# Optimization experiments

Hardware: AMD Instinct MI355X
Metric: run time of the kernel (lower is better)

Reference implementation:

```python
import jax, jax.numpy as jnp
import numpy as np

N_NODES = 50000
N_EDGES = 800000
D = 256          # in_features == out_features == num_classes
T = 4            # number of replicas / linear heads
NS = 64          # num_edges (hyperedges)


def setup_inputs() -> dict:
    key = jax.random.key(0)
    ks = jax.random.split(key, 10)
    s = D ** -0.5
    return {
        "edge_index": jax.random.randint(ks[0], (2, N_EDGES), 0, N_NODES, dtype=jnp.int64)
        if jax.config.jax_enable_x64 else jax.random.randint(ks[0], (2, N_EDGES), 0, N_NODES, dtype=jnp.int32),
        "features": jax.random.normal(ks[1], (N_NODES, D), jnp.float32),
        "lin_w": jax.random.normal(ks[2], (T, D, D), jnp.float32) * s,
        "lin_b": jax.random.normal(ks[3], (T, D), jnp.float32) * 0.01,
        "gcn0_w": jax.random.normal(ks[4], (D, D), jnp.float32) * s,
        "gcn0_b": jax.random.normal(ks[5], (D,), jnp.float32) * 0.01,
        "gcn1_w": jax.random.normal(ks[6], (D, D), jnp.float32) * s,
        "gcn1_b": jax.random.normal(ks[7], (D,), jnp.float32) * 0.01,
        "lin1_w": jax.random.normal(ks[8], (D, NS), jnp.float32) * s,
        "lin1_b": jax.random.normal(ks[9], (NS,), jnp.float32) * 0.01,
    }


def _l2_normalize(x, eps=1e-8):
    n = jnp.sqrt(jnp.sum(x * x, axis=-1, keepdims=True))
    return x / jnp.maximum(n, eps)


def reference(edge_index, features, lin_w, lin_b, gcn0_w, gcn0_b, gcn1_w, gcn1_b, lin1_w, lin1_b):
    num_nodes, d = features.shape
    t = lin_w.shape[0]
    ns = lin1_w.shape[1]
    scale = d ** -0.5  # out_features ** -0.5

    # t linear projections: (t, N, D)
    transformed = jnp.einsum('nd,tdk->tnk', features, lin_w) + lin_b[:, None, :]

    src, dst = edge_index[0], edge_index[1]
    # cosine similarity of features[src] vs each replica's transformed[dst]
    fs = _l2_normalize(features)[src]              # (E, D)
    tf_n = _l2_normalize(transformed)              # (t, N, D)
    sim = jnp.stack([jnp.sum(fs * tf_n[i][dst], axis=-1) for i in range(t)], axis=1)  # (E, t)
    best_idx = jnp.argmax(sim, axis=1)
    best_dst = dst + best_idx.astype(dst.dtype) * num_nodes

    # extra per-replica identity edges: node n -> node n + i*N, i in [0, t)
    ar = jnp.arange(num_nodes, dtype=src.dtype)
    extra_src = jnp.tile(ar, t)
    extra_dst = (ar[None, :] + (jnp.arange(t, dtype=src.dtype) * num_nodes)[:, None]).reshape(-1)

    src_all = jnp.concatenate([src, src, extra_src])
    dst_all = jnp.concatenate([dst, best_dst, extra_dst])
    n_total = (t + 1) * num_nodes

    # PyG gcn_norm: drop pre-existing self loops (weight 0), add one self loop per node,
    # symmetric normalization with degree from destination index.
    loops = jnp.arange(n_total, dtype=src.dtype)
    src2 = jnp.concatenate([src_all, loops])
    dst2 = jnp.concatenate([dst_all, loops])
    w2 = jnp.concatenate([jnp.where(src_all == dst_all, 0.0, 1.0).astype(features.dtype),
                          jnp.ones(n_total, features.dtype)])
    deg = jax.ops.segment_sum(w2, dst2, num_segments=n_total)
    dinv = jnp.where(deg > 0, jax.lax.rsqrt(deg), 0.0)
    norm = w2 * dinv[src2] * dinv[dst2]

    def gcn(x, W, b):
        xw = x @ W
        return jax.ops.segment_sum(norm[:, None] * xw[src2], dst2, num_segments=n_total) + b

    all_features = jnp.concatenate([features, transformed.reshape(t * num_nodes, d)], axis=0)
    # dropout is identity in eval mode
    h = jax.nn.relu(all_features)
    h = gcn(h, gcn0_w, gcn0_b)
    h = jax.nn.relu(h)
    all_features2 = gcn(h, gcn1_w, gcn1_b)          # ((t+1)N, D)
    logits = jax.nn.relu(all_features2) @ lin1_w + lin1_b  # ((t+1)N, NS)

    # H[n, c] counts how many of the (t+1) replicas assign node n to cluster c
    classes = jnp.argmax(logits.reshape(t + 1, num_nodes, ns), axis=-1)  # (t+1, N)
    H = jax.nn.one_hot(classes, ns, dtype=features.dtype).sum(axis=0)     # (N, NS)

    # hyperedge features: sum of all_features2 over base-replica nodes in each hyperedge
    mask = (H > 0).astype(features.dtype)                                  # (N, NS)
    hyperedge_features = mask.T @ all_features2[:num_nodes]                # (NS, D)

    dots = (all_features @ hyperedge_features.T) * scale                   # ((t+1)N, NS)
    return H, hyperedge_features, dots
```

## Files before the change

kernel.cpp:

```cpp
#include <hip/hip_runtime.h>

#define D 256
#define T 4
#define NS 64

typedef unsigned int uint32;
typedef short s16x8 __attribute__((ext_vector_type(8)));
typedef float f32x4 __attribute__((ext_vector_type(4)));

__device__ __forceinline__ float bflo(uint32 u) { return __uint_as_float(u << 16); }
__device__ __forceinline__ float bfhi(uint32 u) { return __uint_as_float(u & 0xffff0000u); }
__device__ __forceinline__ unsigned short f2bf(float x) {
    uint32 u = __float_as_uint(x);
    u = u + 0x7FFFu + ((u >> 16) & 1u);
    return (unsigned short)(u >> 16);
}
__device__ __forceinline__ uint32 pack2(float a, float b) {
    return (uint32)f2bf(a) | ((uint32)f2bf(b) << 16);
}
__device__ __forceinline__ uint32 relu2(uint32 u) {
    uint32 s = u & 0x80008000u;
    uint32 m = ((s >> 15) ^ 0x00010001u) * 0xFFFFu;
    return u & m;
}

__global__ void zero_kernel(uint32* __restrict__ p, long long n)
{
    long long i = (long long)blockIdx.x * blockDim.x + threadIdx.x;
    long long st = (long long)gridDim.x * blockDim.x;
    for (; i < n; i += st) p[i] = 0u;
}

__global__ void f2bf_kernel(const float* __restrict__ in, unsigned short* __restrict__ out,
                            long long n8)
{
    long long i = (long long)blockIdx.x * blockDim.x + threadIdx.x;
    long long st = (long long)gridDim.x * blockDim.x;
    for (; i < n8; i += st) {
        float4 a = *(const float4*)(in + i * 8);
        float4 b = *(const float4*)(in + i * 8 + 4);
        uint4 o;
        o.x = pack2(a.x, a.y); o.y = pack2(a.z, a.w);
        o.z = pack2(b.x, b.y); o.w = pack2(b.z, b.w);
        *(uint4*)(out + i * 8) = o;
    }
}

__global__ void wfrag_kernel(const float* __restrict__ g0, const float* __restrict__ g1,
                             const float* __restrict__ lw, unsigned short* __restrict__ out)
{
    int o = blockIdx.x * 256 + threadIdx.x;
    int mat = blockIdx.y;
    const float* W = (mat == 0) ? g0 : (mat == 1) ? g1 : (lw + (size_t)(mat - 2) * 65536);
    int j = o & 7, lane = (o >> 3) & 63, ks = (o >> 9) & 7, nt = o >> 12;
    int n15 = lane & 15, quad = lane >> 4;
    int k = ks * 32 + quad * 8 + j;
    int n = nt * 16 + n15;
    out[(size_t)mat * 65536 + o] = f2bf(W[(size_t)k * 256 + n]);
}

__global__ __launch_bounds__(256, 2)
void gemm_mfma(const unsigned short* __restrict__ A,
               const unsigned short* __restrict__ Wfrag,
               const float* __restrict__ bias,
               unsigned short* __restrict__ Cout,
               int M, int nStripes)
{
    __shared__ unsigned short Asm[64 * 264];
    int t = threadIdx.x, w = t >> 6, lane = t & 63;
    int n15 = lane & 15, quad = lane >> 4;
    int z = blockIdx.y;
    Wfrag += (size_t)z * 65536;
    bias  += (size_t)z * 256;
    Cout  += (size_t)z * (size_t)M * 256;

    s16x8 bfr[4][8];
#pragma unroll
    for (int nt = 0; nt < 4; nt++)
#pragma unroll
        for (int ks = 0; ks < 8; ks++)
            bfr[nt][ks] = *(const s16x8*)(Wfrag +
                (size_t)(((w * 4 + nt) * 8 + ks) * 64 + lane) * 8);

    float bcol[4];
#pragma unroll
    for (int nt = 0; nt < 4; nt++) bcol[nt] = bias[(w * 4 + nt) * 16 + n15];

    for (int s = blockIdx.x; s < nStripes; s += gridDim.x) {
        int m0 = s * 64;
        __syncthreads();
#pragma unroll
        for (int i = 0; i < 8; i++) {
            int idx = i * 256 + t;
            int m = idx >> 5, kc = (idx & 31) * 8;
            int gm = m0 + m;
            uint4 v = make_uint4(0u, 0u, 0u, 0u);
            if (gm < M) v = *(const uint4*)(A + (size_t)gm * 256 + kc);
            *(uint4*)(Asm + m * 264 + kc) = v;
        }
        __syncthreads();

        f32x4 acc[4][4];
#pragma unroll
        for (int rt = 0; rt < 4; rt++)
#pragma unroll
            for (int nt = 0; nt < 4; nt++)
#pragma unroll
                for (int e = 0; e < 4; e++) acc[rt][nt][e] = 0.f;

#pragma unroll
        for (int rt = 0; rt < 4; rt++) {
            int abase = (rt * 16 + n15) * 264 + quad * 8;
#pragma unroll
            for (int ks = 0; ks < 8; ks++) {
                s16x8 a = *(const s16x8*)(Asm + abase + ks * 32);
#pragma unroll
                for (int nt = 0; nt < 4; nt++)
                    acc[rt][nt] = __builtin_amdgcn_mfma_f32_16x16x32_bf16(
                        a, bfr[nt][ks], acc[rt][nt], 0, 0, 0);
            }
        }

#pragma unroll
        for (int rt = 0; rt < 4; rt++) {
            int row0 = m0 + rt * 16 + quad * 4;
#pragma unroll
            for (int nt = 0; nt < 4; nt++) {
                int colp = (w * 4 + nt) * 16 + n15;
#pragma unroll
                for (int r = 0; r < 4; r++) {
                    int gr = row0 + r;
                    if (gr < M)
                        Cout[(size_t)gr * 256 + colp] = f2bf(acc[rt][nt][r] + bcol[nt]);
                }
            }
        }
    }
}

__global__ __launch_bounds__(256)
void tinv_kernel(const unsigned short* __restrict__ tr, float* __restrict__ tinv, int rows)
{
    int wave = threadIdx.x >> 6, lane = threadIdx.x & 63;
    int r = blockIdx.x * 4 + wave;
    if (r >= rows) return;
    uint2 q = *(const uint2*)(tr + (size_t)r * D + lane * 4);
    float a = bflo(q.x), b = bfhi(q.x), c = bflo(q.y), d = bfhi(q.y);
    float s = a * a + b * b + c * c + d * d;
#pragma unroll
    for (int off = 32; off; off >>= 1) s += __shfl_xor(s, off);
    if (lane == 0) tinv[r] = 1.f / fmaxf(sqrtf(s), 1e-8f);
}

__global__ void ehist_kernel(const int* __restrict__ dst, int* __restrict__ ecnt, int E)
{
    for (int e = blockIdx.x * blockDim.x + threadIdx.x; e < E;
         e += gridDim.x * blockDim.x)
        atomicAdd(ecnt + dst[e], 1);
}

__global__ void escatter_kernel(const int* __restrict__ src, const int* __restrict__ dst,
                                const int* __restrict__ eptr, int* __restrict__ efill,
                                uint2* __restrict__ esorted, int E)
{
    for (int e = blockIdx.x * blockDim.x + threadIdx.x; e < E;
         e += gridDim.x * blockDim.x) {
        int d = dst[e];
        int pos = eptr[d] + atomicAdd(efill + d, 1);
        esorted[pos] = make_uint2((uint32)src[e], (uint32)d);
    }
}

__global__ __launch_bounds__(256)
void sim3_kernel(const uint2* __restrict__ esorted,
                 const unsigned short* __restrict__ featb,
                 const unsigned short* __restrict__ tr, const float* __restrict__ tinv,
                 int* __restrict__ bestS, int E, int Nn)
{
    int w = threadIdx.x >> 6, lane = threadIdx.x & 63;
    int n15 = lane & 15, quad = lane >> 4;
    int base = (blockIdx.x * 4 + w) * 16;
    if (base >= E) return;
    int ei = min(base + n15, E - 1);
    uint2 se = esorted[ei];
    const unsigned short* arow = featb + (size_t)se.x * D + quad * 8;
    const unsigned short* brow = tr + (size_t)se.y * D + quad * 8;
    size_t rstride = (size_t)Nn * D;

    f32x4 a0 = {0.f, 0.f, 0.f, 0.f}, a1 = a0, a2 = a0, a3 = a0;
#pragma unroll
    for (int ks = 0; ks < 8; ks++) {
        s16x8 a  = *(const s16x8*)(arow + ks * 32);
        s16x8 b0 = *(const s16x8*)(brow + ks * 32);
        s16x8 b1 = *(const s16x8*)(brow + rstride + ks * 32);
        s16x8 b2 = *(const s16x8*)(brow + 2 * rstride + ks * 32);
        s16x8 b3 = *(const s16x8*)(brow + 3 * rstride + ks * 32);
        a0 = __builtin_amdgcn_mfma_f32_16x16x32_bf16(a, b0, a0, 0, 0, 0);
        a1 = __builtin_amdgcn_mfma_f32_16x16x32_bf16(a, b1, a1, 0, 0, 0);
        a2 = __builtin_amdgcn_mfma_f32_16x16x32_bf16(a, b2, a2, 0, 0, 0);
        a3 = __builtin_amdgcn_mfma_f32_16x16x32_bf16(a, b3, a3, 0, 0, 0);
    }
    if (quad == (n15 >> 2) && base + n15 < E) {
        int r = n15 & 3;
        int d = (int)se.y;
        float v0 = a0[r] * tinv[d];
        float v1 = a1[r] * tinv[Nn + d];
        float v2 = a2[r] * tinv[2 * Nn + d];
        float v3 = a3[r] * tinv[3 * Nn + d];
        float bv = v0; int bi = 0;
        if (v1 > bv) { bv = v1; bi = 1; }
        if (v2 > bv) { bv = v2; bi = 2; }
        if (v3 > bv) { bv = v3; bi = 3; }
        bestS[base + n15] = bi;
    }
}

__device__ __forceinline__ void decode_edge(int e, const uint2* __restrict__ esorted,
                                            const int* __restrict__ bestS,
                                            int E, int Nn, int& s, int& d, bool& keep)
{
    if (e < E) {
        uint2 se = esorted[e];
        s = (int)se.x; d = (int)se.y; keep = (s != d);
    } else if (e < 2 * E) {
        int k = e - E;
        uint2 se = esorted[k];
        s = (int)se.x; d = (int)se.y + bestS[k] * Nn; keep = (s != d);
    } else if (e < 2 * E + T * Nn) {
        int k = e - 2 * E; int i = k / Nn; int n = k - i * Nn;
        s = n; d = n + i * Nn; keep = (i != 0);
    } else {
        int v = e - (2 * E + T * Nn); s = v; d = v; keep = true;
    }
}

__global__ void hist_kernel(const uint2* __restrict__ esorted, const int* __restrict__ bestS,
                            int* __restrict__ cnt, int E, int Nn)
{
    int total = 2 * E + (2 * T + 1) * Nn;
    for (int e = blockIdx.x * blockDim.x + threadIdx.x; e < total;
         e += gridDim.x * blockDim.x) {
        int s, d; bool keep;
        decode_edge(e, esorted, bestS, E, Nn, s, d, keep);
        if (keep) atomicAdd(cnt + d, 1);
    }
}

__global__ void dinv_kernel(const int* __restrict__ cnt, float* __restrict__ dinv, int n)
{
    int v = blockIdx.x * blockDim.x + threadIdx.x;
    if (v < n) dinv[v] = (cnt[v] > 0) ? rsqrtf((float)cnt[v]) : 0.f;
}

__global__ void emeta_kernel(const uint2* __restrict__ esorted, const int* __restrict__ bestS,
                             const float* __restrict__ dinv, uint2* __restrict__ emeta, int E)
{
    for (int e = blockIdx.x * blockDim.x + threadIdx.x; e < E;
         e += gridDim.x * blockDim.x) {
        uint2 se = esorted[e];
        uint32 packed = se.x | ((uint32)bestS[e] << 27);
        emeta[e] = make_uint2(packed, __float_as_uint(dinv[se.x]));
    }
}

__global__ void scan_sums(const int* __restrict__ cnt, int* __restrict__ aux, int n)
{
    __shared__ int sd[256];
    int idx = blockIdx.x * 256 + threadIdx.x;
    sd[threadIdx.x] = (idx < n) ? cnt[idx] : 0;
    __syncthreads();
    for (int off = 128; off; off >>= 1) {
        if (threadIdx.x < off) sd[threadIdx.x] += sd[threadIdx.x + off];
        __syncthreads();
    }
    if (threadIdx.x == 0) aux[blockIdx.x] = sd[0];
}

__global__ void scan_aux(const int* __restrict__ aux, int* __restrict__ auxex, int nb)
{
    __shared__ int sd[1024];
    int t = threadIdx.x;
    int v = (t < nb) ? aux[t] : 0;
    sd[t] = v;
    __syncthreads();
    for (int off = 1; off < 1024; off <<= 1) {
        int x = (t >= off) ? sd[t - off] : 0;
        __syncthreads();
        sd[t] += x;
        __syncthreads();
    }
    if (t < nb) auxex[t] = sd[t] - v;
}

__global__ void scan_write(const int* __restrict__ cnt, const int* __restrict__ auxex,
                           int* __restrict__ rowptr, int n)
{
    __shared__ int sd[256];
    int t = threadIdx.x;
    int idx = blockIdx.x * 256 + t;
    int v = (idx < n) ? cnt[idx] : 0;
    sd[t] = v;
    __syncthreads();
    for (int off = 1; off < 256; off <<= 1) {
        int x = (t >= off) ? sd[t - off] : 0;
        __syncthreads();
        sd[t] += x;
        __syncthreads();
    }
    if (idx < n) {
        int rp = auxex[blockIdx.x] + sd[t] - v;
        rowptr[idx] = rp;
        if (idx == n - 1) rowptr[n] = rp + v;
    }
}

__global__ __launch_bounds__(256)
void agg5_kernel(const int* __restrict__ eptr, const uint2* __restrict__ emeta,
                 const unsigned short* __restrict__ xa,
                 const unsigned short* __restrict__ xb,
                 const float* __restrict__ dinv,
                 unsigned short* __restrict__ outb, int Nn)
{
    int wave = threadIdx.x >> 6, lane = threadIdx.x & 63;
    int v = blockIdx.x * 4 + wave;
    if (v >= Nn) return;

    float dv  = dinv[v];
    float dr1 = dinv[v + Nn];
    float dr2 = dinv[v + 2 * Nn];
    float dr3 = dinv[v + 3 * Nn];
    float dr4 = dinv[v + 4 * Nn];

    uint2 qv = *(const uint2*)(xa + (size_t)v * D + lane * 4);
    qv.x = relu2(qv.x); qv.y = relu2(qv.y);
    float y0 = bflo(qv.x), y1 = bfhi(qv.x), y2 = bflo(qv.y), y3 = bfhi(qv.y);

    float wsb = dv * dv;
    float b0 = wsb * y0, b1 = wsb * y1, b2 = wsb * y2, b3 = wsb * y3;

    float wi1 = dv * dr1, wi2 = dv * dr2, wi3 = dv * dr3;
    float r10 = wi1 * y0, r11 = wi1 * y1, r12 = wi1 * y2, r13 = wi1 * y3;
    float r20 = wi2 * y0, r21 = wi2 * y1, r22 = wi2 * y2, r23 = wi2 * y3;
    float r30 = wi3 * y0, r31 = wi3 * y1, r32 = wi3 * y2, r33 = wi3 * y3;
    float r40 = 0.f, r41 = 0.f, r42 = 0.f, r43 = 0.f;

    {
        uint2 q = *(const uint2*)(xb + ((size_t)0 * Nn + v) * D + lane * 4);
        q.x = relu2(q.x); q.y = relu2(q.y);
        float ws = dr1 * dr1;
        r10 = fmaf(ws, bflo(q.x), r10); r11 = fmaf(ws, bfhi(q.x), r11);
        r12 = fmaf(ws, bflo(q.y), r12); r13 = fmaf(ws, bfhi(q.y), r13);
    }
    {
        uint2 q = *(const uint2*)(xb + ((size_t)1 * Nn + v) * D + lane * 4);
        q.x = relu2(q.x); q.y = relu2(q.y);
        float ws = dr2 * dr2;
        r20 = fmaf(ws, bflo(q.x), r20); r21 = fmaf(ws, bfhi(q.x), r21);
        r22 = fmaf(ws, bflo(q.y), r22); r23 = fmaf(ws, bfhi(q.y), r23);
    }
    {
        uint2 q = *(const uint2*)(xb + ((size_t)2 * Nn + v) * D + lane * 4);
        q.x = relu2(q.x); q.y = relu2(q.y);
        float ws = dr3 * dr3;
        r30 = fmaf(ws, bflo(q.x), r30); r31 = fmaf(ws, bfhi(q.x), r31);
        r32 = fmaf(ws, bflo(q.y), r32); r33 = fmaf(ws, bfhi(q.y), r33);
    }
    {
        uint2 q = *(const uint2*)(xb + ((size_t)3 * Nn + v) * D + lane * 4);
        q.x = relu2(q.x); q.y = relu2(q.y);
        float ws = dr4 * dr4;
        r40 = fmaf(ws, bflo(q.x), r40); r41 = fmaf(ws, bfhi(q.x), r41);
        r42 = fmaf(ws, bflo(q.y), r42); r43 = fmaf(ws, bfhi(q.y), r43);
    }

    int j = eptr[v], jend = eptr[v + 1];

#define EDGE_BODY(qq, ss, bb, ww)                                                  \
    {                                                                              \
        float x0 = bflo(qq.x), x1 = bfhi(qq.x), x2 = bflo(qq.y), x3 = bfhi(qq.y);  \
        float wb = (ss != v) ? (ww) * dv : 0.f;                                    \
        if (bb == 0) wb += wb;                                                     \
        b0 = fmaf(wb, x0, b0); b1 = fmaf(wb, x1, b1);                              \
        b2 = fmaf(wb, x2, b2); b3 = fmaf(wb, x3, b3);                              \
        if (bb == 1) {                                                             \
            float wr = (ww) * dr1;                                                 \
            r10 = fmaf(wr, x0, r10); r11 = fmaf(wr, x1, r11);                      \
            r12 = fmaf(wr, x2, r12); r13 = fmaf(wr, x3, r13);                      \
        } else if (bb == 2) {                                                      \
            float wr = (ww) * dr2;                                                 \
            r20 = fmaf(wr, x0, r20); r21 = fmaf(wr, x1, r21);                      \
            r22 = fmaf(wr, x2, r22); r23 = fmaf(wr, x3, r23);                      \
        } else if (bb == 3) {                                                      \
            float wr = (ww) * dr3;                                                 \
            r30 = fmaf(wr, x0, r30); r31 = fmaf(wr, x1, r31);                      \
            r32 = fmaf(wr, x2, r32); r33 = fmaf(wr, x3, r33);                      \
        }                                                                          \
    }

    for (; j + 2 <= jend; j += 2) {
        uint2 m0 = emeta[j];
        uint2 m1 = emeta[j + 1];
        uint32 su0 = (uint32)__builtin_amdgcn_readfirstlane((int)m0.x);
        uint32 su1 = (uint32)__builtin_amdgcn_readfirstlane((int)m1.x);
        float ws0 = __uint_as_float((uint32)__builtin_amdgcn_readfirstlane((int)m0.y));
        float ws1 = __uint_as_float((uint32)__builtin_amdgcn_readfirstlane((int)m1.y));
        int s0 = (int)(su0 & 0x07FFFFFFu), bx0 = (int)(su0 >> 27);
        int s1 = (int)(su1 & 0x07FFFFFFu), bx1 = (int)(su1 >> 27);
        uint2 q0 = *(const uint2*)(xa + (size_t)s0 * D + lane * 4);
        uint2 q1 = *(const uint2*)(xa + (size_t)s1 * D + lane * 4);
        q0.x = relu2(q0.x); q0.y = relu2(q0.y);
        q1.x = relu2(q1.x); q1.y = relu2(q1.y);
        EDGE_BODY(q0, s0, bx0, ws0);
        EDGE_BODY(q1, s1, bx1, ws1);
    }
    if (j < jend) {
        uint2 m0 = emeta[j];
        uint32 su0 = (uint32)__builtin_amdgcn_readfirstlane((int)m0.x);
        float ws0 = __uint_as_float((uint32)__builtin_amdgcn_readfirstlane((int)m0.y));
        int s0 = (int)(su0 & 0x07FFFFFFu), bx0 = (int)(su0 >> 27);
        uint2 q0 = *(const uint2*)(xa + (size_t)s0 * D + lane * 4);
        q0.x = relu2(q0.x); q0.y = relu2(q0.y);
        EDGE_BODY(q0, s0, bx0, ws0);
    }
#undef EDGE_BODY

    uint2 o;
    o.x = pack2(b0, b1); o.y = pack2(b2, b3);
    *(uint2*)(outb + (size_t)v * D + lane * 4) = o;
    o.x = pack2(r10, r11); o.y = pack2(r12, r13);
    *(uint2*)(outb + ((size_t)v + Nn) * D + lane * 4) = o;
    o.x = pack2(r20, r21); o.y = pack2(r22, r23);
    *(uint2*)(outb + ((size_t)v + 2 * (size_t)Nn) * D + lane * 4) = o;
    o.x = pack2(r30, r31); o.y = pack2(r32, r33);
    *(uint2*)(outb + ((size_t)v + 3 * (size_t)Nn) * D + lane * 4) = o;
    o.x = pack2(r40, r41); o.y = pack2(r42, r43);
    *(uint2*)(outb + ((size_t)v + 4 * (size_t)Nn) * D + lane * 4) = o;
}

__global__ __launch_bounds__(256, 2)
void logits_mfma(const unsigned short* __restrict__ af2, const float* __restrict__ Wl,
                 const float* __restrict__ bl, float* __restrict__ H,
                 int M, int Nn, int nStripes)
{
    __shared__ unsigned short Asm[64 * 264];
    int t = threadIdx.x, w = t >> 6, lane = t & 63;
    int n15 = lane & 15, quad = lane >> 4;

    s16x8 bfr[4][8];
#pragma unroll
    for (int nt = 0; nt < 4; nt++)
#pragma unroll
        for (int ks = 0; ks < 8; ks++) {
            s16x8 f;
#pragma unroll
            for (int j = 0; j < 8; j++) {
                int k = ks * 32 + quad * 8 + j;
                f[j] = (short)f2bf(Wl[(size_t)k * NS + nt * 16 + n15]);
            }
            bfr[nt][ks] = f;
        }
    float bcol[4];
#pragma unroll
    for (int nt = 0; nt < 4; nt++) bcol[nt] = bl[nt * 16 + n15];

    for (int s = blockIdx.x; s < nStripes; s += gridDim.x) {
        int m0 = s * 64;
        __syncthreads();
#pragma unroll
        for (int i = 0; i < 8; i++) {
            int idx = i * 256 + t;
            int m = idx >> 5, kc = (idx & 31) * 8;
            int gm = m0 + m;
            uint4 v = make_uint4(0u, 0u, 0u, 0u);
            if (gm < M) {
                v = *(const uint4*)(af2 + (size_t)gm * 256 + kc);
                v.x = relu2(v.x); v.y = relu2(v.y);
                v.z = relu2(v.z); v.w = relu2(v.w);
            }
            *(uint4*)(Asm + m * 264 + kc) = v;
        }
        __syncthreads();

        f32x4 acc[4];
#pragma unroll
        for (int nt = 0; nt < 4; nt++)
#pragma unroll
            for (int e = 0; e < 4; e++) acc[nt][e] = 0.f;

        int abase = (w * 16 + n15) * 264 + quad * 8;
#pragma unroll
        for (int ks = 0; ks < 8; ks++) {
            s16x8 a = *(const s16x8*)(Asm + abase + ks * 32);
#pragma unroll
            for (int nt = 0; nt < 4; nt++)
                acc[nt] = __builtin_amdgcn_mfma_f32_16x16x32_bf16(
                    a, bfr[nt][ks], acc[nt], 0, 0, 0);
        }

#pragma unroll
        for (int e = 0; e < 4; e++) {
            float bv = acc[0][e] + bcol[0]; int bi = n15;
#pragma unroll
            for (int nt = 1; nt < 4; nt++) {
                float v = acc[nt][e] + bcol[nt];
                int c = nt * 16 + n15;
                if (v > bv) { bv = v; bi = c; }
            }
#pragma unroll
            for (int off = 1; off < 16; off <<= 1) {
                float ov = __shfl_xor(bv, off);
                int   oi = __shfl_xor(bi, off);
                if (ov > bv || (ov == bv && oi < bi)) { bv = ov; bi = oi; }
            }
            if (n15 == 0) {
                int gr = m0 + w * 16 + quad * 4 + e;
                if (gr < M) atomicAdd(H + (size_t)(gr % Nn) * NS + bi, 1.0f);
            }
        }
    }
}

__global__ __launch_bounds__(256)
void he3_kernel(const float* __restrict__ H, const unsigned short* __restrict__ af2,
                float* __restrict__ he, int Nn)
{
    __shared__ float acc[NS * 128];
    int t = threadIdx.x, w = t >> 6, lane = t & 63;
    int half = blockIdx.y;

    for (int i = t * 4; i < NS * 128; i += 1024)
        *(float4*)(acc + i) = make_float4(0.f, 0.f, 0.f, 0.f);
    __syncthreads();

    int n0 = blockIdx.x * 512 + w * 128;
    int n1 = min(n0 + 128, Nn);
    const unsigned short* xbase = af2 + half * 128 + lane * 2;

    if (n0 < n1) {
        float hv = H[(size_t)n0 * NS + lane];
        uint32 xr = *(const uint32*)(xbase + (size_t)n0 * D);
        for (int n = n0; n < n1; n++) {
            float chv = hv;
            uint32 cx = xr;
            if (n + 1 < n1) {
                hv = H[(size_t)(n + 1) * NS + lane];
                xr = *(const uint32*)(xbase + (size_t)(n + 1) * D);
            }
            unsigned long long m = __ballot(chv > 0.f);
            float x0 = bflo(cx), x1 = bfhi(cx);
            while (m) {
                int c = __ffsll(m) - 1;
                m &= m - 1;
                float* p = acc + c * 128 + lane * 2;
                atomicAdd(p, x0);
                atomicAdd(p + 1, x1);
            }
        }
    }
    __syncthreads();

    for (int i = t; i < NS * 128; i += 256) {
        int c = i >> 7, f = i & 127;
        atomicAdd(he + (size_t)c * D + half * 128 + f, acc[i]);
    }
}

__global__ void bigb_copy(const float* __restrict__ he, float* __restrict__ BigB)
{
    int idx = blockIdx.x * 256 + threadIdx.x;
    if (idx < D * NS) {
        int d = idx >> 6, c = idx & 63;
        BigB[idx] = he[(size_t)c * D + d];
    }
}

__global__ __launch_bounds__(256)
void bigb_mm(const float* __restrict__ lin_w, const float* __restrict__ lin_b,
             const float* __restrict__ he, float* __restrict__ BigB,
             float* __restrict__ beta)
{
    int gw = (int)((blockIdx.x * 256 + threadIdx.x) >> 6);
    int lane = threadIdx.x & 63;
    const int totalA = T * D * NS;
    if (gw >= totalA + T * NS) return;
    const float* xrow; const float* hrow; float* outp;
    if (gw < totalA) {
        int t = gw / (D * NS); int rem = gw - t * D * NS;
        int d = rem / NS; int c = rem - d * NS;
        xrow = lin_w + ((size_t)t * D + d) * D;
        hrow = he + (size_t)c * D;
        outp = BigB + ((size_t)(t + 1) * D + d) * NS + c;
    } else {
        int i = gw - totalA; int t = i / NS; int c = i - t * NS;
        xrow = lin_b + (size_t)t * D;
        hrow = he + (size_t)c * D;
        outp = beta + (size_t)(t + 1) * NS + c;
    }
    float4 x = *(const float4*)(xrow + lane * 4);
    float4 h = *(const float4*)(hrow + lane * 4);
    float s = x.x * h.x + x.y * h.y + x.z * h.z + x.w * h.w;
#pragma unroll
    for (int off = 32; off; off >>= 1) s += __shfl_xor(s, off);
    if (lane == 0) *outp = s;
}

__global__ __launch_bounds__(256, 2)
void dots_mfma(const unsigned short* __restrict__ featb,
               const float* __restrict__ feat32, int useBf,
               const float* __restrict__ BigB,
               const float* __restrict__ beta, float* __restrict__ dots,
               int Nn, int nStripes)
{
    __shared__ unsigned short Asm[64 * 264];
    int t = threadIdx.x, w = t >> 6, lane = t & 63;
    int n15 = lane & 15, quad = lane >> 4;
    int rho = blockIdx.y;
    const float* Bp = BigB + (size_t)rho * D * NS;

    s16x8 bfr[4][8];
#pragma unroll
    for (int nt = 0; nt < 4; nt++)
#pragma unroll
        for (int ks = 0; ks < 8; ks++) {
            s16x8 f;
#pragma unroll
            for (int j = 0; j < 8; j++) {
                int k = ks * 32 + quad * 8 + j;
                f[j] = (short)f2bf(Bp[(size_t)k * NS + nt * 16 + n15]);
            }
            bfr[nt][ks] = f;
        }
    float bcol[4];
#pragma unroll
    for (int nt = 0; nt < 4; nt++) bcol[nt] = beta[rho * NS + nt * 16 + n15];

    for (int s = blockIdx.x; s < nStripes; s += gridDim.x) {
        int m0 = s * 64;
        __syncthreads();
#pragma unroll
        for (int i = 0; i < 8; i++) {
            int idx = i * 256 + t;
            int m = idx >> 5, kc = (idx & 31) * 8;
            int gm = m0 + m;
            uint4 o = make_uint4(0u, 0u, 0u, 0u);
            if (gm < Nn) {
                if (useBf) {
                    o = *(const uint4*)(featb + (size_t)gm * 256 + kc);
                } else {
                    float4 a = *(const float4*)(feat32 + (size_t)gm * 256 + kc);
                    float4 b = *(const float4*)(feat32 + (size_t)gm * 256 + kc + 4);
                    o.x = pack2(a.x, a.y); o.y = pack2(a.z, a.w);
                    o.z = pack2(b.x, b.y); o.w = pack2(b.z, b.w);
                }
            }
            *(uint4*)(Asm + m * 264 + kc) = o;
        }
        __syncthreads();

        f32x4 acc[4];
#pragma unroll
        for (int nt = 0; nt < 4; nt++)
#pragma unroll
            for (int e = 0; e < 4; e++) acc[nt][e] = 0.f;

        int abase = (w * 16 + n15) * 264 + quad * 8;
#pragma unroll
        for (int ks = 0; ks < 8; ks++) {
            s16x8 a = *(const s16x8*)(Asm + abase + ks * 32);
#pragma unroll
            for (int nt = 0; nt < 4; nt++)
                acc[nt] = __builtin_amdgcn_mfma_f32_16x16x32_bf16(
                    a, bfr[nt][ks], acc[nt], 0, 0, 0);
        }

#pragma unroll
        for (int e = 0; e < 4; e++) {
            int gr = m0 + w * 16 + quad * 4 + e;
            if (gr >= Nn) continue;
#pragma unroll
            for (int nt = 0; nt < 4; nt++) {
                int c = nt * 16 + n15;
                dots[((size_t)rho * Nn + gr) * NS + c] = (acc[nt][e] + bcol[nt]) * 0.0625f;
            }
        }
    }
}

extern "C" void kernel_launch(void* const* d_in, const int* in_sizes, int n_in,
                              void* d_out, int out_size, void* d_ws, size_t ws_size,
                              hipStream_t stream)
{
    const int*   edge_index = (const int*)d_in[0];
    const float* features   = (const float*)d_in[1];
    const float* lin_w      = (const float*)d_in[2];
    const float* lin_b      = (const float*)d_in[3];
    const float* gcn0_w     = (const float*)d_in[4];
    const float* gcn0_b     = (const float*)d_in[5];
    const float* gcn1_w     = (const float*)d_in[6];
    const float* gcn1_b     = (const float*)d_in[7];
    const float* lin1_w     = (const float*)d_in[8];
    const float* lin1_b     = (const float*)d_in[9];

    int E  = in_sizes[0] / 2;
    int Nn = in_sizes[1] / D;
    int n_total = (T + 1) * Nn;
    int Mrep = T * Nn;

    const int* src = edge_index;
    const int* dst = edge_index + E;

    float* out_H    = (float*)d_out;
    float* out_he   = out_H + (size_t)Nn * NS;
    float* out_dots = out_he + (size_t)NS * D;

    char* ws0 = (char*)d_ws;
    char* wsp = ws0;
    auto carve = [&](size_t bytes) {
        char* p = wsp; wsp += (bytes + 255) & ~(size_t)255; return p;
    };
    unsigned short* R1   = (unsigned short*)carve((size_t)n_total * D * 2);
    unsigned short* R2   = (unsigned short*)carve((size_t)n_total * D * 2);
    float*          BigB = (float*)carve((size_t)(T + 1) * D * NS * 4);
    float*          beta = (float*)carve((size_t)(T + 1) * NS * 4);
    unsigned short* transformed = R2;

    size_t featb_bytes = (size_t)Nn * D * 2;
    unsigned short* featb = nullptr;
    int useBfDots = 0;
    if ((size_t)(wsp - ws0) + featb_bytes + 256 <= ws_size) {
        featb = (unsigned short*)carve(featb_bytes);
        useBfDots = 1;
    }

    char* sc = (char*)out_dots;
    auto carve2 = [&](size_t bytes) {
        char* p = sc; sc += (bytes + 255) & ~(size_t)255; return p;
    };
    float* tinv    = (float*)carve2((size_t)Mrep * 4);
    int*   best    = (int*)carve2((size_t)E * 4);
    int*   cnt     = (int*)carve2((size_t)n_total * 4);
    float* dinv    = (float*)carve2((size_t)n_total * 4);
    int*   aux     = (int*)carve2(1024 * 4);
    int*   auxex   = (int*)carve2(1024 * 4);
    if (!featb) featb = (unsigned short*)carve2(featb_bytes);
    unsigned short* Wfrags = (unsigned short*)carve2((size_t)6 * 65536 * 2);
    int*   ecnt    = (int*)carve2((size_t)Nn * 4);
    int*   eptr    = (int*)carve2((size_t)(Nn + 1) * 4);
    int*   efill   = (int*)carve2((size_t)Nn * 4);
    uint2* esorted = (uint2*)carve2((size_t)E * 8);
    uint2* emeta   = (uint2*)carve2((size_t)E * 8);

    zero_kernel<<<512, 256, 0, stream>>>((uint32*)cnt, n_total);
    zero_kernel<<<512, 256, 0, stream>>>((uint32*)ecnt, Nn);
    zero_kernel<<<512, 256, 0, stream>>>((uint32*)efill, Nn);
    zero_kernel<<<512, 256, 0, stream>>>((uint32*)out_H, (long long)Nn * NS + NS * D);
    zero_kernel<<<1, 256, 0, stream>>>((uint32*)beta, (T + 1) * NS);

    wfrag_kernel<<<dim3(256, 6), 256, 0, stream>>>(gcn0_w, gcn1_w, lin_w, Wfrags);
    f2bf_kernel<<<2048, 256, 0, stream>>>(features, featb, (long long)Nn * D / 8);

    int strN = (Nn + 63) / 64;
    gemm_mfma<<<dim3(512, T), 256, 0, stream>>>(featb, Wfrags + 2 * 65536, lin_b,
                                                transformed, Nn, strN);
    tinv_kernel<<<(Mrep + 3) / 4, 256, 0, stream>>>(transformed, tinv, Mrep);

    ehist_kernel<<<2048, 256, 0, stream>>>(dst, ecnt, E);
    int enb = (Nn + 255) / 256;
    scan_sums<<<enb, 256, 0, stream>>>(ecnt, aux, Nn);
    scan_aux<<<1, 1024, 0, stream>>>(aux, auxex, enb);
    scan_write<<<enb, 256, 0, stream>>>(ecnt, auxex, eptr, Nn);
    escatter_kernel<<<2048, 256, 0, stream>>>(src, dst, eptr, efill, esorted, E);
    int nGroups = (E + 15) / 16;
    sim3_kernel<<<(nGroups + 3) / 4, 256, 0, stream>>>(esorted, featb, transformed,
                                                       tinv, best, E, Nn);

    hist_kernel<<<2048, 256, 0, stream>>>(esorted, best, cnt, E, Nn);
    dinv_kernel<<<(n_total + 255) / 256, 256, 0, stream>>>(cnt, dinv, n_total);
    emeta_kernel<<<2048, 256, 0, stream>>>(esorted, best, dinv, emeta, E);

    int strT = (n_total + 63) / 64;
    agg5_kernel<<<(Nn + 3) / 4, 256, 0, stream>>>(eptr, emeta, featb, transformed,
                                                  dinv, R1, Nn);
    gemm_mfma<<<dim3(512, 1), 256, 0, stream>>>(R1, Wfrags, gcn0_b, R1, n_total, strT);

    agg5_kernel<<<(Nn + 3) / 4, 256, 0, stream>>>(eptr, emeta, R1, R1 + (size_t)Nn * D,
                                                  dinv, R2, Nn);
    gemm_mfma<<<dim3(512, 1), 256, 0, stream>>>(R2, Wfrags + 65536, gcn1_b, R2,
                                                n_total, strT);

    logits_mfma<<<512, 256, 0, stream>>>(R2, lin1_w, lin1_b, out_H, n_total, Nn, strT);

    he3_kernel<<<dim3((Nn + 511) / 512, 2), 256, 0, stream>>>(out_H, R2, out_he, Nn);

    bigb_copy<<<(D * NS + 255) / 256, 256, 0, stream>>>(out_he, BigB);
    bigb_mm<<<(T * D * NS + T * NS + 3) / 4, 256, 0, stream>>>(lin_w, lin_b, out_he,
                                                               BigB, beta);
    dots_mfma<<<dim3(160, 5), 256, 0, stream>>>(featb, features, useBfDots,
                                                BigB, beta, out_dots, Nn, strN);
}
```

Before: 1.072 ms.

## Split hyperedge accumulation into smaller chunks with two-stage partial reduction

The hyperedge-feature kernel now gives each wave 32 nodes instead of 128, which launches about four times as many blocks and exposes more parallelism over the sequential per-node loop. Each block writes its shared-memory accumulator to a per-block partial buffer, reusing the R1 scratch, instead of issuing global atomics. A new reduction kernel sums the partials in 8 slices and finishes with far fewer atomics. In exchange it adds extra global memory traffic for the partial buffers and one more kernel launch.

```diff
diff --git a/kernel.cpp b/kernel.cpp
--- a/kernel.cpp
+++ b/kernel.cpp
@@ -520,9 +520,10 @@
     }
 }
 
+#define HE_CHUNK 32
 __global__ __launch_bounds__(256)
-void he3_kernel(const float* __restrict__ H, const unsigned short* __restrict__ af2,
-                float* __restrict__ he, int Nn)
+void he4_kernel(const float* __restrict__ H, const unsigned short* __restrict__ af2,
+                float* __restrict__ partials, int Nn, int NB)
 {
     __shared__ float acc[NS * 128];
     int t = threadIdx.x, w = t >> 6, lane = t & 63;
@@ -532,8 +533,8 @@
         *(float4*)(acc + i) = make_float4(0.f, 0.f, 0.f, 0.f);
     __syncthreads();
 
-    int n0 = blockIdx.x * 512 + w * 128;
-    int n1 = min(n0 + 128, Nn);
+    int n0 = blockIdx.x * (4 * HE_CHUNK) + w * HE_CHUNK;
+    int n1 = min(n0 + HE_CHUNK, Nn);
     const unsigned short* xbase = af2 + half * 128 + lane * 2;
 
     if (n0 < n1) {
@@ -559,10 +560,24 @@
     }
     __syncthreads();
 
-    for (int i = t; i < NS * 128; i += 256) {
-        int c = i >> 7, f = i & 127;
-        atomicAdd(he + (size_t)c * D + half * 128 + f, acc[i]);
-    }
+    float* pdst = partials + ((size_t)half * NB + blockIdx.x) * (NS * 128);
+    for (int i = t * 4; i < NS * 128; i += 1024)
+        *(float4*)(pdst + i) = *(const float4*)(acc + i);
+}
+
+__global__ __launch_bounds__(256)
+void he_reduce(const float* __restrict__ partials, float* __restrict__ he,
+               int NB, int sliceB)
+{
+    int idx = blockIdx.x * 256 + threadIdx.x;
+    int half = idx >> 13, r = idx & 8191;
+    int c = r >> 7, f = r & 127;
+    int b0 = blockIdx.y * sliceB;
+    int b1 = min(b0 + sliceB, NB);
+    float s = 0.f;
+    for (int b = b0; b < b1; b++)
+        s += partials[((size_t)half * NB + b) * 8192 + r];
+    atomicAdd(he + (size_t)c * D + half * 128 + f, s);
 }
 
 __global__ void bigb_copy(const float* __restrict__ he, float* __restrict__ BigB)
@@ -750,6 +765,9 @@
     uint2* esorted = (uint2*)carve2((size_t)E * 8);
     uint2* emeta   = (uint2*)carve2((size_t)E * 8);
 
+    int NB = (Nn + 4 * HE_CHUNK - 1) / (4 * HE_CHUNK);
+    float* partials = (float*)R1;
+
     zero_kernel<<<512, 256, 0, stream>>>((uint32*)cnt, n_total);
     zero_kernel<<<512, 256, 0, stream>>>((uint32*)ecnt, Nn);
     zero_kernel<<<512, 256, 0, stream>>>((uint32*)efill, Nn);
@@ -790,7 +808,9 @@
 
     logits_mfma<<<512, 256, 0, stream>>>(R2, lin1_w, lin1_b, out_H, n_total, Nn, strT);
 
-    he3_kernel<<<dim3((Nn + 511) / 512, 2), 256, 0, stream>>>(out_H, R2, out_he, Nn);
+    he4_kernel<<<dim3(NB, 2), 256, 0, stream>>>(out_H, R2, partials, Nn, NB);
+    int sliceB = (NB + 7) / 8;
+    he_reduce<<<dim3(64, 8), 256, 0, stream>>>(partials, out_he, NB, sliceB);
 
     bigb_copy<<<(D * NS + 255) / 256, 256, 0, stream>>>(out_he, BigB);
     bigb_mm<<<(T * D * NS + T * NS + 3) / 4, 256, 0, stream>>>(lin_w, lin_b, out_he,
```

Result: no change. 1.077 ms (+0.5%).

## Compute hyperedge features as bf16 MFMA GEMM with transposed mask

Applied to the files above, without the earlier changes.

Replaces the ballot-and-LDS-atomic hyperedge accumulation with three kernels: one builds a transposed bf16 0/1 mask from H, one runs a split-K MFMA GEMM of mask^T times the bf16 all_features2 rows into per-block partials, and one reduces the partials into the output. This removes the serialized per-cluster shared-memory atomics and the global atomics, at the cost of two extra launches and partial-buffer traffic. The GEMM reads af2 rows up to the padded K length, which can run past Nn when Nn is not a multiple of 256; those rows are multiplied by zero mask entries.

```diff
diff --git a/kernel.cpp b/kernel.cpp
--- a/kernel.cpp
+++ b/kernel.cpp
@@ -521,48 +521,102 @@
 }
 
 __global__ __launch_bounds__(256)
-void he3_kernel(const float* __restrict__ H, const unsigned short* __restrict__ af2,
-                float* __restrict__ he, int Nn)
-{
-    __shared__ float acc[NS * 128];
+void maskTb_kernel(const float* __restrict__ H, unsigned short* __restrict__ maskTb,
+                   int Nn, int Kpad)
+{
+    __shared__ unsigned short tile[64 * 72];
+    int t = threadIdx.x;
+    int n0 = blockIdx.x * 64;
+    int c = t & 63, rr = t >> 6;
+#pragma unroll
+    for (int i = 0; i < 16; i++) {
+        int n = rr + i * 4;
+        float hv = (n0 + n < Nn) ? H[(size_t)(n0 + n) * NS + c] : 0.f;
+        tile[c * 72 + n] = (hv > 0.f) ? (unsigned short)0x3F80 : (unsigned short)0;
+    }
+    __syncthreads();
+#pragma unroll
+    for (int i = 0; i < 4; i++) {
+        int idx = i * 256 + t;
+        int cc = idx >> 4, ch = idx & 15;
+        if (idx < 512) {
+            cc = idx >> 3; ch = idx & 7;
+            uint4 v = *(const uint4*)(tile + cc * 72 + ch * 8);
+            *(uint4*)(maskTb + (size_t)cc * Kpad + n0 + ch * 8) = v;
+        }
+    }
+}
+
+__global__ __launch_bounds__(256, 2)
+void he_gemm(const unsigned short* __restrict__ maskTb,
+             const unsigned short* __restrict__ af2,
+             float* __restrict__ partials, int Kpad)
+{
+    __shared__ unsigned short Bsm[32 * 264];
     int t = threadIdx.x, w = t >> 6, lane = t & 63;
-    int half = blockIdx.y;
-
-    for (int i = t * 4; i < NS * 128; i += 1024)
-        *(float4*)(acc + i) = make_float4(0.f, 0.f, 0.f, 0.f);
-    __syncthreads();
-
-    int n0 = blockIdx.x * 512 + w * 128;
-    int n1 = min(n0 + 128, Nn);
-    const unsigned short* xbase = af2 + half * 128 + lane * 2;
-
-    if (n0 < n1) {
-        float hv = H[(size_t)n0 * NS + lane];
-        uint32 xr = *(const uint32*)(xbase + (size_t)n0 * D);
-        for (int n = n0; n < n1; n++) {
-            float chv = hv;
-            uint32 cx = xr;
-            if (n + 1 < n1) {
-                hv = H[(size_t)(n + 1) * NS + lane];
-                xr = *(const uint32*)(xbase + (size_t)(n + 1) * D);
-            }
-            unsigned long long m = __ballot(chv > 0.f);
-            float x0 = bflo(cx), x1 = bfhi(cx);
-            while (m) {
-                int c = __ffsll(m) - 1;
-                m &= m - 1;
-                float* p = acc + c * 128 + lane * 2;
-                atomicAdd(p, x0);
-                atomicAdd(p + 1, x1);
-            }
-        }
-    }
-    __syncthreads();
-
-    for (int i = t; i < NS * 128; i += 256) {
-        int c = i >> 7, f = i & 127;
-        atomicAdd(he + (size_t)c * D + half * 128 + f, acc[i]);
-    }
+    int n15 = lane & 15, quad = lane >> 4;
+    int k0 = blockIdx.x * 256;
+
+    f32x4 acc[4][4];
+#pragma unroll
+    for (int mt = 0; mt < 4; mt++)
+#pragma unroll
+        for (int nt = 0; nt < 4; nt++)
+#pragma unroll
+            for (int e = 0; e < 4; e++) acc[mt][nt][e] = 0.f;
+
+    for (int s = 0; s < 8; s++) {
+        int k = k0 + s * 32;
+        __syncthreads();
+#pragma unroll
+        for (int i = 0; i < 4; i++) {
+            int idx = i * 256 + t;
+            int row = idx >> 5, col8 = (idx & 31) * 8;
+            uint4 v = *(const uint4*)(af2 + (size_t)(k + row) * 256 + col8);
+            *(uint4*)(Bsm + row * 264 + col8) = v;
+        }
+        __syncthreads();
+
+        s16x8 a[4];
+#pragma unroll
+        for (int mt = 0; mt < 4; mt++)
+            a[mt] = *(const s16x8*)(maskTb + (size_t)(mt * 16 + n15) * Kpad
+                                    + k + quad * 8);
+#pragma unroll
+        for (int nt = 0; nt < 4; nt++) {
+            int ncol = w * 64 + nt * 16 + n15;
+            s16x8 b;
+#pragma unroll
+            for (int j = 0; j < 8; j++)
+                b[j] = (short)Bsm[(quad * 8 + j) * 264 + ncol];
+#pragma unroll
+            for (int mt = 0; mt < 4; mt++)
+                acc[mt][nt] = __builtin_amdgcn_mfma_f32_16x16x32_bf16(
+                    a[mt], b, acc[mt][nt], 0, 0, 0);
+        }
+    }
+
+    float* pdst = partials + (size_t)blockIdx.x * (64 * 256);
+#pragma unroll
+    for (int mt = 0; mt < 4; mt++)
+#pragma unroll
+        for (int nt = 0; nt < 4; nt++)
+#pragma unroll
+            for (int r = 0; r < 4; r++) {
+                int m = mt * 16 + quad * 4 + r;
+                int n = w * 64 + nt * 16 + n15;
+                pdst[(size_t)m * 256 + n] = acc[mt][nt][r];
+            }
+}
+
+__global__ __launch_bounds__(256)
+void he_reduce2(const float* __restrict__ partials, float* __restrict__ he, int KB)
+{
+    int idx = blockIdx.x * 256 + threadIdx.x;
+    float s = 0.f;
+    for (int b = 0; b < KB; b++)
+        s += partials[(size_t)b * 16384 + idx];
+    he[idx] = s;
 }
 
 __global__ void bigb_copy(const float* __restrict__ he, float* __restrict__ BigB)
@@ -712,6 +766,9 @@
     float* out_H    = (float*)d_out;
     float* out_he   = out_H + (size_t)Nn * NS;
     float* out_dots = out_he + (size_t)NS * D;
+
+    int KB   = (Nn + 255) / 256;
+    int Kpad = KB * 256;
 
     char* ws0 = (char*)d_ws;
     char* wsp = ws0;
@@ -749,6 +806,9 @@
     int*   efill   = (int*)carve2((size_t)Nn * 4);
     uint2* esorted = (uint2*)carve2((size_t)E * 8);
     uint2* emeta   = (uint2*)carve2((size_t)E * 8);
+    unsigned short* maskTb = (unsigned short*)carve2((size_t)NS * Kpad * 2);
+
+    float* partials = (float*)R1;
 
     zero_kernel<<<512, 256, 0, stream>>>((uint32*)cnt, n_total);
     zero_kernel<<<512, 256, 0, stream>>>((uint32*)ecnt, Nn);
@@ -790,7 +850,9 @@
 
     logits_mfma<<<512, 256, 0, stream>>>(R2, lin1_w, lin1_b, out_H, n_total, Nn, strT);
 
-    he3_kernel<<<dim3((Nn + 511) / 512, 2), 256, 0, stream>>>(out_H, R2, out_he, Nn);
+    maskTb_kernel<<<Kpad / 64, 256, 0, stream>>>(out_H, maskTb, Nn, Kpad);
+    he_gemm<<<KB, 256, 0, stream>>>(maskTb, R2, partials, Kpad);
+    he_reduce2<<<64, 256, 0, stream>>>(partials, out_he, KB);
 
     bigb_copy<<<(D * NS + 255) / 256, 256, 0, stream>>>(out_he, BigB);
     bigb_mm<<<(T * D * NS + T * NS + 3) / 4, 256, 0, stream>>>(lin_w, lin_b, out_he,
```

Result: faster. 1.005 ms (-6.2%).
